# Optimization experiments

Measured on AMD Instinct MI355X. Metric: run time of the kernel, lower is better.

## Reference

```python
import jax, jax.numpy as jnp
import numpy as np

EPS = 1e-06
NEG_SLOPE = 0.2
B, N, CIN = 2, 2048, 64
QK, V, H = 128, 128, 8


def ev_nonlin(x, w1, b1, w2, b2):
    # EVNNonLinearity with skip_connection == 1, leaky_relu
    norm = jnp.linalg.norm(x, axis=-2, keepdims=True)  # [..., 1, nf]
    zero_norm = norm <= EPS
    norm = norm + EPS
    h = jax.nn.leaky_relu(norm @ w1 + b1, NEG_SLOPE)
    norm_bn = (h @ w2 + b2) + norm
    return jnp.where(zero_norm, x, x / norm * norm_bn)


def ev_layernorm(x):
    x_norm = jnp.linalg.norm(x, axis=-2, keepdims=True)
    sigma = jnp.std(jnp.concatenate([x_norm, -x_norm], -1), axis=-1, keepdims=True)
    return x / (sigma + EPS)


def setup_inputs() -> dict:
    key = jax.random.key(0)
    ks = jax.random.split(key, 20)
    def w(k, *shape):
        fan_in = shape[0]
        return jax.random.normal(k, shape, jnp.float32) / np.sqrt(fan_in)
    hd_qk = QK // H
    hd_v = V // H
    return {
        'qfts': jax.random.normal(ks[0], (B, N, 3, CIN), jnp.float32),
        'kvfts': jax.random.normal(ks[1], (B, N, 3, CIN), jnp.float32),
        # EVLinearLeakyReLU for q branch
        'w_q_in': w(ks[2], CIN, QK),
        'q_nl_w1': w(ks[3], QK, QK // 2), 'q_nl_b1': jnp.zeros((QK // 2,), jnp.float32),
        'q_nl_w2': w(ks[4], QK // 2, QK), 'q_nl_b2': jnp.zeros((QK,), jnp.float32),
        # EVLinearLeakyReLU for kv branch
        'w_kv_in': w(ks[5], CIN, QK),
        'kv_nl_w1': w(ks[6], QK, QK // 2), 'kv_nl_b1': jnp.zeros((QK // 2,), jnp.float32),
        'kv_nl_w2': w(ks[7], QK // 2, QK), 'kv_nl_b2': jnp.zeros((QK,), jnp.float32),
        # DenseGeneral projections (no bias)
        'w_q': w(ks[8], QK, H, hd_qk),
        'w_k': w(ks[9], QK, H, hd_qk),
        'w_v': w(ks[10], QK, H, hd_v),
        # output EVLinearLeakyReLU
        'w_out': w(ks[11], V, V),
        'o_nl_w1': w(ks[12], V, V // 2), 'o_nl_b1': jnp.zeros((V // 2,), jnp.float32),
        'o_nl_w2': w(ks[13], V // 2, V), 'o_nl_b2': jnp.zeros((V,), jnp.float32),
    }


def reference(qfts, kvfts, w_q_in, q_nl_w1, q_nl_b1, q_nl_w2, q_nl_b2,
              w_kv_in, kv_nl_w1, kv_nl_b1, kv_nl_w2, kv_nl_b2,
              w_q, w_k, w_v, w_out, o_nl_w1, o_nl_b1, o_nl_w2, o_nl_b2):
    # EVLinearLeakyReLU on q and kv features: [b,n,3,cin] -> [b,n,3,qk]
    qf = ev_nonlin(qfts @ w_q_in, q_nl_w1, q_nl_b1, q_nl_w2, q_nl_b2)
    kf = ev_nonlin(kvfts @ w_kv_in, kv_nl_w1, kv_nl_b1, kv_nl_w2, kv_nl_b2)
    # DenseGeneral to heads, then heads to front: [h,b,n,3,d]
    q = jnp.einsum('bnfc,chd->hbnfd', qf, w_q)
    k = jnp.einsum('bnfc,chd->hbnfd', kf, w_k)
    v = jnp.einsum('bnfc,chd->hbnfd', kf, w_v)
    # normalize_qk
    q = ev_layernorm(q)
    k = ev_layernorm(k)
    # dot attention: contract vector(3) and head_dim axes
    scale = np.sqrt(k.shape[-1]).astype(np.float32)
    attn = jnp.einsum('hbqfd,hbkfd->hbqk', q, k)
    attn = jax.nn.softmax(attn / scale, axis=-1)
    resi = jnp.einsum('hbqk,hbkfd->hbqfd', attn, v)
    # 'h b q f d -> b q f (h d)'
    h, b, nq, f, d = resi.shape
    resi = jnp.moveaxis(resi, 0, 3).reshape(b, nq, f, h * d)
    # output EVLinearLeakyReLU
    out = ev_nonlin(resi @ w_out, o_nl_w1, o_nl_b1, o_nl_w2, o_nl_b2)
    return out
```

## Files before the change

### kernel.cpp

```cpp
#include <hip/hip_runtime.h>
#include <math.h>

#define EPSV 1e-6f
#define NSL  0.2f
#define BB   2
#define NN   2048
#define HH   8
#define TBP  16

typedef short bf16x8 __attribute__((ext_vector_type(8)));
typedef float f32x4  __attribute__((ext_vector_type(4)));

__device__ __forceinline__ unsigned cvt_pk_bf16(float a, float b) {
  unsigned r;
  asm("v_cvt_pk_bf16_f32 %0, %1, %2" : "=v"(r) : "v"(a), "v"(b));
  return r;
}
__device__ __forceinline__ float u2f(unsigned u) {
  union { unsigned u; float f; } v; v.u = u; return v.f;
}
__device__ __forceinline__ float leaky(float a) { return a > 0.f ? a : NSL * a; }

__device__ __forceinline__ void pack8(float4 a, float4 b, uint4& hi, uint4& lo) {
  hi.x = cvt_pk_bf16(a.x, a.y);
  hi.y = cvt_pk_bf16(a.z, a.w);
  hi.z = cvt_pk_bf16(b.x, b.y);
  hi.w = cvt_pk_bf16(b.z, b.w);
  float d0 = a.x - u2f(hi.x << 16), d1 = a.y - u2f(hi.x & 0xffff0000u);
  float d2 = a.z - u2f(hi.y << 16), d3 = a.w - u2f(hi.y & 0xffff0000u);
  float d4 = b.x - u2f(hi.z << 16), d5 = b.y - u2f(hi.z & 0xffff0000u);
  float d6 = b.z - u2f(hi.w << 16), d7 = b.w - u2f(hi.w & 0xffff0000u);
  lo.x = cvt_pk_bf16(d0, d1);
  lo.y = cvt_pk_bf16(d2, d3);
  lo.z = cvt_pk_bf16(d4, d5);
  lo.w = cvt_pk_bf16(d6, d7);
}

__global__ __launch_bounds__(64) void wconv_kernel(
    const float* __restrict__ wq_in, const float* __restrict__ qw1, const float* __restrict__ qw2,
    const float* __restrict__ wkv_in, const float* __restrict__ kw1, const float* __restrict__ kw2,
    const float* __restrict__ w_q, const float* __restrict__ w_k, const float* __restrict__ w_v,
    const float* __restrict__ w_out, const float* __restrict__ ow1, const float* __restrict__ ow2,
    unsigned short* __restrict__ WB)
{
  const int b = blockIdx.x;
  const int lane = threadIdx.x;
  const float* src; int N, toff;
  if      (b < 16)  { src = wq_in;  N = 128; toff = b; }
  else if (b < 32)  { src = qw1;    N = 64;  toff = b - 16; }
  else if (b < 48)  { src = qw2;    N = 128; toff = b - 32; }
  else if (b < 64)  { src = wkv_in; N = 128; toff = b - 48; }
  else if (b < 80)  { src = kw1;    N = 64;  toff = b - 64; }
  else if (b < 96)  { src = kw2;    N = 128; toff = b - 80; }
  else if (b < 128) { src = w_q;    N = 128; toff = b - 96; }
  else if (b < 160) { src = w_k;    N = 128; toff = b - 128; }
  else if (b < 192) { src = w_v;    N = 128; toff = b - 160; }
  else if (b < 224) { src = w_out;  N = 128; toff = b - 192; }
  else if (b < 240) { src = ow1;    N = 64;  toff = b - 224; }
  else              { src = ow2;    N = 128; toff = b - 240; }
  const int NT = N >> 4;
  const int kk = toff / NT, nj = toff % NT;
  const int k0 = kk * 32 + (lane >> 4) * 8;
  const int ch = nj * 16 + (lane & 15);
  float vals[8];
  #pragma unroll
  for (int j = 0; j < 8; ++j) vals[j] = src[(size_t)(k0 + j) * N + ch];
  float4 a = {vals[0], vals[1], vals[2], vals[3]};
  float4 bb = {vals[4], vals[5], vals[6], vals[7]};
  uint4 hi, lo;
  pack8(a, bb, hi, lo);
  unsigned short* dst = WB + (size_t)b * 1024;
  *(uint4*)(dst + lane * 8) = hi;
  *(uint4*)(dst + 512 + lane * 8) = lo;
}


__global__ __launch_bounds__(256) void pre_kernel(
    const float* __restrict__ qfts, const float* __restrict__ kvfts,
    const float* __restrict__ qb1, const float* __restrict__ qb2,
    const float* __restrict__ kb1, const float* __restrict__ kb2,
    const unsigned short* __restrict__ WB,
    unsigned short* __restrict__ QW, unsigned short* __restrict__ KW, unsigned short* __restrict__ VW)
{
  const bool is_kv = blockIdx.y != 0;
  const float* x_in = is_kv ? kvfts : qfts;
  const float* b1 = is_kv ? kb1 : qb1;
  const float* b2 = is_kv ? kb2 : qb2;
  unsigned short* FW = is_kv ? KW : QW;
  const float ln_sc = is_kv ? 1.f : 0.25f * 1.44269504088896f;
  const int tb_in = is_kv ? 48 : 0;
  const int tb_w1 = is_kv ? 64 : 16;
  const int tb_w2 = is_kv ? 80 : 32;
  const int tb_p  = is_kv ? 128 : 96;

  const int t0 = blockIdx.x * TBP;
  const int tid = threadIdx.x;
  const int wv = tid >> 6, lane = tid & 63;
  const int col = lane & 15, kg = lane >> 4;
  const int nj0 = wv * 2;
  const int n0 = t0 & (NN - 1), bsel = t0 >> 11;

  __shared__ __align__(16) char smem[50688];
  float* xs       = (float*)smem;
  float* norm_lds = (float*)(smem + 12544);
  float* h_lds    = (float*)(smem + 20992);
  float* f_lds    = (float*)(smem + 25344);
  float* stage    = (float*)smem;

  {
    const float4* src = (const float4*)(x_in + (size_t)t0 * 192);
    #pragma unroll
    for (int i = 0; i < 3; ++i) {
      int idx = tid + i * 256;
      int row = idx / 48, c4 = idx % 48;
      *(float4*)&xs[row * 196 + c4 * 4] = src[idx];
    }
  }
  __syncthreads();

  f32x4 pacc[3][2];
  #pragma unroll
  for (int mf = 0; mf < 3; ++mf)
    #pragma unroll
    for (int njl = 0; njl < 2; ++njl) pacc[mf][njl] = (f32x4){0.f, 0.f, 0.f, 0.f};
  {
    bf16x8 axh[3][2], axl[3][2];
    #pragma unroll
    for (int mf = 0; mf < 3; ++mf)
      #pragma unroll
      for (int kk = 0; kk < 2; ++kk) {
        const float* pa = &xs[col * 196 + mf * 64 + kk * 32 + kg * 8];
        uint4 hi, lo;
        pack8(*(const float4*)pa, *(const float4*)(pa + 4), hi, lo);
        axh[mf][kk] = *(bf16x8*)&hi; axl[mf][kk] = *(bf16x8*)&lo;
      }
    #pragma unroll
    for (int kk = 0; kk < 2; ++kk)
      #pragma unroll
      for (int njl = 0; njl < 2; ++njl) {
        const unsigned short* wb = WB + (size_t)(tb_in + kk * 8 + nj0 + njl) * 1024 + lane * 8;
        bf16x8 bh = *(const bf16x8*)wb;
        bf16x8 bl = *(const bf16x8*)(wb + 512);
        #pragma unroll
        for (int mf = 0; mf < 3; ++mf) {
          pacc[mf][njl] = __builtin_amdgcn_mfma_f32_16x16x32_bf16(axh[mf][kk], bh, pacc[mf][njl], 0, 0, 0);
          pacc[mf][njl] = __builtin_amdgcn_mfma_f32_16x16x32_bf16(axh[mf][kk], bl, pacc[mf][njl], 0, 0, 0);
          pacc[mf][njl] = __builtin_amdgcn_mfma_f32_16x16x32_bf16(axl[mf][kk], bh, pacc[mf][njl], 0, 0, 0);
        }
      }
  }

  f32x4 np4[2]; int zm = 0;
  #pragma unroll
  for (int njl = 0; njl < 2; ++njl) {
    f32x4 ss = pacc[0][njl] * pacc[0][njl] + pacc[1][njl] * pacc[1][njl] + pacc[2][njl] * pacc[2][njl];
    #pragma unroll
    for (int i = 0; i < 4; ++i) {
      float nn = sqrtf(ss[i]);
      if (nn <= EPSV) zm |= 1 << (njl * 4 + i);
      np4[njl][i] = nn + EPSV;
      norm_lds[(kg * 4 + i) * 132 + (nj0 + njl) * 16 + col] = np4[njl][i];
    }
  }
  __syncthreads();

  {
    f32x4 hacc = {0.f, 0.f, 0.f, 0.f};
    #pragma unroll
    for (int kk = 0; kk < 4; ++kk) {
      const float* pa = &norm_lds[col * 132 + kk * 32 + kg * 8];
      uint4 hi, lo;
      pack8(*(const float4*)pa, *(const float4*)(pa + 4), hi, lo);
      bf16x8 ah = *(bf16x8*)&hi, al = *(bf16x8*)&lo;
      const unsigned short* wb = WB + (size_t)(tb_w1 + kk * 4 + wv) * 1024 + lane * 8;
      bf16x8 bh = *(const bf16x8*)wb, bl = *(const bf16x8*)(wb + 512);
      hacc = __builtin_amdgcn_mfma_f32_16x16x32_bf16(ah, bh, hacc, 0, 0, 0);
      hacc = __builtin_amdgcn_mfma_f32_16x16x32_bf16(ah, bl, hacc, 0, 0, 0);
      hacc = __builtin_amdgcn_mfma_f32_16x16x32_bf16(al, bh, hacc, 0, 0, 0);
    }
    float b1v = b1[wv * 16 + col];
    #pragma unroll
    for (int i = 0; i < 4; ++i)
      h_lds[(kg * 4 + i) * 68 + wv * 16 + col] = leaky(hacc[i] + b1v);
  }
  __syncthreads();

  {
    f32x4 bna[2] = {{0.f, 0.f, 0.f, 0.f}, {0.f, 0.f, 0.f, 0.f}};
    #pragma unroll
    for (int kk = 0; kk < 2; ++kk) {
      const float* pa = &h_lds[col * 68 + kk * 32 + kg * 8];
      uint4 hi, lo;
      pack8(*(const float4*)pa, *(const float4*)(pa + 4), hi, lo);
      bf16x8 ah = *(bf16x8*)&hi, al = *(bf16x8*)&lo;
      #pragma unroll
      for (int njl = 0; njl < 2; ++njl) {
        const unsigned short* wb = WB + (size_t)(tb_w2 + kk * 8 + nj0 + njl) * 1024 + lane * 8;
        bf16x8 bh = *(const bf16x8*)wb, bl = *(const bf16x8*)(wb + 512);
        bna[njl] = __builtin_amdgcn_mfma_f32_16x16x32_bf16(ah, bh, bna[njl], 0, 0, 0);
        bna[njl] = __builtin_amdgcn_mfma_f32_16x16x32_bf16(ah, bl, bna[njl], 0, 0, 0);
        bna[njl] = __builtin_amdgcn_mfma_f32_16x16x32_bf16(al, bh, bna[njl], 0, 0, 0);
      }
    }
    #pragma unroll
    for (int njl = 0; njl < 2; ++njl) {
      float b2v = b2[(nj0 + njl) * 16 + col];
      #pragma unroll
      for (int i = 0; i < 4; ++i) {
        float r = (zm >> (njl * 4 + i)) & 1 ? 1.f
                 : (bna[njl][i] + b2v + np4[njl][i]) / np4[njl][i];
        #pragma unroll
        for (int mf = 0; mf < 3; ++mf)
          f_lds[(mf * 16 + kg * 4 + i) * 132 + (nj0 + njl) * 16 + col] = pacc[mf][njl][i] * r;
      }
    }
  }
  __syncthreads();

  f32x4 qacc[3][2], vacc[3][2];
  #pragma unroll
  for (int mf = 0; mf < 3; ++mf)
    #pragma unroll
    for (int njl = 0; njl < 2; ++njl) {
      qacc[mf][njl] = (f32x4){0.f, 0.f, 0.f, 0.f};
      vacc[mf][njl] = (f32x4){0.f, 0.f, 0.f, 0.f};
    }
  #pragma unroll
  for (int kk = 0; kk < 4; ++kk) {
    bf16x8 afh[3], afl[3];
    #pragma unroll
    for (int mf = 0; mf < 3; ++mf) {
      const float* pa = &f_lds[(mf * 16 + col) * 132 + kk * 32 + kg * 8];
      uint4 hi, lo;
      pack8(*(const float4*)pa, *(const float4*)(pa + 4), hi, lo);
      afh[mf] = *(bf16x8*)&hi; afl[mf] = *(bf16x8*)&lo;
    }
    #pragma unroll
    for (int njl = 0; njl < 2; ++njl) {
      const unsigned short* wbq = WB + (size_t)(tb_p + kk * 8 + nj0 + njl) * 1024 + lane * 8;
      bf16x8 qbh = *(const bf16x8*)wbq, qbl = *(const bf16x8*)(wbq + 512);
      #pragma unroll
      for (int mf = 0; mf < 3; ++mf) {
        qacc[mf][njl] = __builtin_amdgcn_mfma_f32_16x16x32_bf16(afh[mf], qbh, qacc[mf][njl], 0, 0, 0);
        qacc[mf][njl] = __builtin_amdgcn_mfma_f32_16x16x32_bf16(afh[mf], qbl, qacc[mf][njl], 0, 0, 0);
        qacc[mf][njl] = __builtin_amdgcn_mfma_f32_16x16x32_bf16(afl[mf], qbh, qacc[mf][njl], 0, 0, 0);
      }
      if (is_kv) {
        const unsigned short* wbv = WB + (size_t)(160 + kk * 8 + nj0 + njl) * 1024 + lane * 8;
        bf16x8 vbh = *(const bf16x8*)wbv, vbl = *(const bf16x8*)(wbv + 512);
        #pragma unroll
        for (int mf = 0; mf < 3; ++mf) {
          vacc[mf][njl] = __builtin_amdgcn_mfma_f32_16x16x32_bf16(afh[mf], vbh, vacc[mf][njl], 0, 0, 0);
          vacc[mf][njl] = __builtin_amdgcn_mfma_f32_16x16x32_bf16(afh[mf], vbl, vacc[mf][njl], 0, 0, 0);
          vacc[mf][njl] = __builtin_amdgcn_mfma_f32_16x16x32_bf16(afl[mf], vbh, vacc[mf][njl], 0, 0, 0);
        }
      }
    }
  }
  __syncthreads();

  #pragma unroll
  for (int njl = 0; njl < 2; ++njl) {
    #pragma unroll
    for (int i = 0; i < 4; ++i) {
      float ss = qacc[0][njl][i] * qacc[0][njl][i]
               + qacc[1][njl][i] * qacc[1][njl][i]
               + qacc[2][njl][i] * qacc[2][njl][i];
      ss += __shfl_xor(ss, 1, 16);
      ss += __shfl_xor(ss, 2, 16);
      ss += __shfl_xor(ss, 4, 16);
      ss += __shfl_xor(ss, 8, 16);
      float inv = ln_sc / (sqrtf(ss * (1.f / 16.f)) + EPSV);
      const int tl = kg * 4 + i;
      #pragma unroll
      for (int mf = 0; mf < 3; ++mf)
        stage[tl * 388 + mf * 128 + (nj0 + njl) * 16 + col] = qacc[mf][njl][i] * inv;
    }
  }
  __syncthreads();

  {
    const int f0 = lane >> 5;
    const int ddb = ((lane >> 4) & 1) * 8;
    const int row = lane & 15;
    #pragma unroll
    for (int h2 = 0; h2 < 2; ++h2) {
      const int hh = wv * 2 + h2;
      const int hbw = hh * BB + bsel;
      const size_t basew = (size_t)(hbw * 128 + (n0 >> 4)) * 1536;
      {
        const float* p0 = stage + row * 388 + f0 * 128 + hh * 16 + ddb;
        uint4 hi, lo;
        pack8(*(const float4*)p0, *(const float4*)(p0 + 4), hi, lo);
        *(uint4*)(FW + basew + lane * 8) = hi;
        *(uint4*)(FW + basew + 768 + lane * 8) = lo;
      }
      if (lane < 32) {
        const float* p1 = stage + row * 388 + 2 * 128 + hh * 16 + ddb;
        uint4 hi, lo;
        pack8(*(const float4*)p1, *(const float4*)(p1 + 4), hi, lo);
        *(uint4*)(FW + basew + 512 + lane * 8) = hi;
        *(uint4*)(FW + basew + 768 + 512 + lane * 8) = lo;
      }
    }
  }

  if (is_kv) {
    __syncthreads();
    #pragma unroll
    for (int njl = 0; njl < 2; ++njl)
      #pragma unroll
      for (int mf = 0; mf < 3; ++mf)
        #pragma unroll
        for (int i = 0; i < 4; ++i)
          stage[mf * 2112 + (kg * 4 + i) * 132 + (nj0 + njl) * 16 + col] = vacc[mf][njl][i];
    __syncthreads();

    const int s0 = (n0 >> 3) & 3;
    if (lane < 32) {
      const int seg = lane;
      const int tlb = (seg >> 4) * 8;
      const int dd = seg & 15;
      #pragma unroll
      for (int h2 = 0; h2 < 2; ++h2) {
        const int hh = wv * 2 + h2;
        const int hbw = hh * BB + bsel;
        #pragma unroll
        for (int f = 0; f < 3; ++f) {
          const size_t vbase = (size_t)((hbw * 64 + (n0 >> 5)) * 3 + f) * 1024;
          float vals[8];
          #pragma unroll
          for (int j = 0; j < 8; ++j)
            vals[j] = stage[f * 2112 + (tlb + j) * 132 + hh * 16 + dd];
          float4 a = {vals[0], vals[1], vals[2], vals[3]};
          float4 b = {vals[4], vals[5], vals[6], vals[7]};
          uint4 hi, lo;
          pack8(a, b, hi, lo);
          *(uint4*)(VW + vbase + (size_t)(s0 * 16 + seg) * 8) = hi;
          *(uint4*)(VW + vbase + 512 + (size_t)(s0 * 16 + seg) * 8) = lo;
        }
      }
    }
  }
}

#define THR 10.0f

__global__ __launch_bounds__(512, 4) void attn_kernel(
    const unsigned short* __restrict__ QW, const unsigned short* __restrict__ KW,
    const unsigned short* __restrict__ VW, float* __restrict__ Ob)
{
  const int lane = threadIdx.x & 63;
  const int w = threadIdx.x >> 6;
  const int qt = w & 1;
  const int kq = w >> 1;
  const int hb = blockIdx.y;
  const int tA = blockIdx.x * 4 + qt * 2;
  const int q = lane & 15, g = lane >> 4;

  __shared__ unsigned short plds[8][2][1152];
  float* comb = (float*)plds;

  bf16x8 qh0[2], ql0[2], qh1[2], ql1[2];
  #pragma unroll
  for (int qs = 0; qs < 2; ++qs) {
    const size_t qbase = (size_t)(hb * 128 + tA + qs) * 1536;
    qh0[qs] = *(const bf16x8*)(QW + qbase + lane * 8);
    ql0[qs] = *(const bf16x8*)(QW + qbase + 768 + lane * 8);
    qh1[qs] = (bf16x8){0,0,0,0,0,0,0,0};
    ql1[qs] = (bf16x8){0,0,0,0,0,0,0,0};
    if (lane < 32) {
      qh1[qs] = *(const bf16x8*)(QW + qbase + 512 + lane * 8);
      ql1[qs] = *(const bf16x8*)(QW + qbase + 768 + 512 + lane * 8);
    }
  }

  f32x4 o[2][3];
  #pragma unroll
  for (int qs = 0; qs < 2; ++qs)
    #pragma unroll
    for (int f = 0; f < 3; ++f) o[qs][f] = (f32x4){0.f, 0.f, 0.f, 0.f};
  float m[2] = {-INFINITY, -INFINITY}, l[2] = {0.f, 0.f};

  for (int T = kq * 8; T < kq * 8 + 8; ++T) {
    f32x4 sc[2][4];
    __builtin_amdgcn_s_setprio(1);
    #pragma unroll
    for (int st = 0; st < 4; ++st) {
      const size_t kb = (size_t)(hb * 128 + T * 4 + st) * 1536;
      bf16x8 kh0 = *(const bf16x8*)(KW + kb + lane * 8);
      bf16x8 kl0 = *(const bf16x8*)(KW + kb + 768 + lane * 8);
      bf16x8 kh1 = *(const bf16x8*)(KW + kb + 512 + lane * 8);
      bf16x8 kl1 = *(const bf16x8*)(KW + kb + 768 + 512 + lane * 8);
      #pragma unroll
      for (int qs = 0; qs < 2; ++qs) {
        f32x4 a = {0.f, 0.f, 0.f, 0.f};
        a = __builtin_amdgcn_mfma_f32_16x16x32_bf16(kh0, qh0[qs], a, 0, 0, 0);
        a = __builtin_amdgcn_mfma_f32_16x16x32_bf16(kh0, ql0[qs], a, 0, 0, 0);
        a = __builtin_amdgcn_mfma_f32_16x16x32_bf16(kl0, qh0[qs], a, 0, 0, 0);
        a = __builtin_amdgcn_mfma_f32_16x16x32_bf16(kh1, qh1[qs], a, 0, 0, 0);
        a = __builtin_amdgcn_mfma_f32_16x16x32_bf16(kh1, ql1[qs], a, 0, 0, 0);
        a = __builtin_amdgcn_mfma_f32_16x16x32_bf16(kl1, qh1[qs], a, 0, 0, 0);
        sc[qs][st] = a;
      }
    }
    __builtin_amdgcn_s_setprio(0);

    bf16x8 v0h[3], v0l[3];
    {
      const int kc0 = T * 2;
      #pragma unroll
      for (int f = 0; f < 3; ++f) {
        const size_t vb = (size_t)((hb * 64 + kc0) * 3 + f) * 1024;
        v0h[f] = *(const bf16x8*)(VW + vb + lane * 8);
        v0l[f] = *(const bf16x8*)(VW + vb + 512 + lane * 8);
      }
    }

    #pragma unroll
    for (int qs = 0; qs < 2; ++qs) {
      float tm = sc[qs][0][0];
      #pragma unroll
      for (int st = 0; st < 4; ++st)
        #pragma unroll
        for (int r = 0; r < 4; ++r) tm = fmaxf(tm, sc[qs][st][r]);
      tm = fmaxf(tm, __shfl_xor(tm, 16));
      tm = fmaxf(tm, __shfl_xor(tm, 32));
      if (__any(tm > m[qs] + THR)) {
        float mnew = fmaxf(m[qs], tm);
        float scl = __builtin_amdgcn_exp2f(m[qs] - mnew);
        l[qs] *= scl;
        #pragma unroll
        for (int f = 0; f < 3; ++f) {
          o[qs][f][0] *= scl; o[qs][f][1] *= scl;
          o[qs][f][2] *= scl; o[qs][f][3] *= scl;
        }
        m[qs] = mnew;
      }
      float lp = 0.f;
      #pragma unroll
      for (int st = 0; st < 4; ++st) {
        float p0 = __builtin_amdgcn_exp2f(sc[qs][st][0] - m[qs]);
        float p1 = __builtin_amdgcn_exp2f(sc[qs][st][1] - m[qs]);
        float p2 = __builtin_amdgcn_exp2f(sc[qs][st][2] - m[qs]);
        float p3 = __builtin_amdgcn_exp2f(sc[qs][st][3] - m[qs]);
        lp += (p0 + p1) + (p2 + p3);
        uint2 uh = {cvt_pk_bf16(p0, p1), cvt_pk_bf16(p2, p3)};
        *(uint2*)&plds[w][qs][q * 72 + st * 16 + g * 4] = uh;
      }
      lp += __shfl_xor(lp, 16);
      lp += __shfl_xor(lp, 32);
      l[qs] += lp;
    }

    asm volatile("s_waitcnt lgkmcnt(0)" ::: "memory");

    __builtin_amdgcn_s_setprio(1);
    {
      bf16x8 pb[2];
      #pragma unroll
      for (int qs = 0; qs < 2; ++qs)
        pb[qs] = *(const bf16x8*)&plds[w][qs][q * 72 + g * 8];
      #pragma unroll
      for (int f = 0; f < 3; ++f)
        #pragma unroll
        for (int qs = 0; qs < 2; ++qs) {
          o[qs][f] = __builtin_amdgcn_mfma_f32_16x16x32_bf16(v0h[f], pb[qs], o[qs][f], 0, 0, 0);
          o[qs][f] = __builtin_amdgcn_mfma_f32_16x16x32_bf16(v0l[f], pb[qs], o[qs][f], 0, 0, 0);
        }
    }
    {
      const int kc = T * 2 + 1;
      bf16x8 pb[2];
      #pragma unroll
      for (int qs = 0; qs < 2; ++qs)
        pb[qs] = *(const bf16x8*)&plds[w][qs][q * 72 + 32 + g * 8];
      #pragma unroll
      for (int f = 0; f < 3; ++f) {
        const size_t vb = (size_t)((hb * 64 + kc) * 3 + f) * 1024;
        bf16x8 vh = *(const bf16x8*)(VW + vb + lane * 8);
        bf16x8 vl = *(const bf16x8*)(VW + vb + 512 + lane * 8);
        #pragma unroll
        for (int qs = 0; qs < 2; ++qs) {
          o[qs][f] = __builtin_amdgcn_mfma_f32_16x16x32_bf16(vh, pb[qs], o[qs][f], 0, 0, 0);
          o[qs][f] = __builtin_amdgcn_mfma_f32_16x16x32_bf16(vl, pb[qs], o[qs][f], 0, 0, 0);
        }
      }
    }
    __builtin_amdgcn_s_setprio(0);
  }

  #define SLOT(qt_, qs_, r_) (comb + ((((qt_) * 2 + (qs_)) * 2 + (r_)) * 64 + lane) * 14)
  __syncthreads();
  if (kq & 1) {
    #pragma unroll
    for (int qs = 0; qs < 2; ++qs) {
      float* cb = SLOT(qt, qs, kq >> 1);
      #pragma unroll
      for (int f = 0; f < 3; ++f)
        #pragma unroll
        for (int r = 0; r < 4; ++r) cb[f * 4 + r] = o[qs][f][r];
      cb[12] = m[qs]; cb[13] = l[qs];
    }
  }
  __syncthreads();
  if (!(kq & 1)) {
    #pragma unroll
    for (int qs = 0; qs < 2; ++qs) {
      const float* cb = SLOT(qt, qs, kq >> 1);
      float m1 = cb[12], l1 = cb[13];
      float mn = fmaxf(m[qs], m1);
      float s0 = __builtin_amdgcn_exp2f(m[qs] - mn);
      float s1 = __builtin_amdgcn_exp2f(m1 - mn);
      l[qs] = l[qs] * s0 + l1 * s1;
      #pragma unroll
      for (int f = 0; f < 3; ++f)
        #pragma unroll
        for (int r = 0; r < 4; ++r)
          o[qs][f][r] = o[qs][f][r] * s0 + cb[f * 4 + r] * s1;
      m[qs] = mn;
    }
  }
  __syncthreads();
  if (kq == 2) {
    #pragma unroll
    for (int qs = 0; qs < 2; ++qs) {
      float* cb = SLOT(qt, qs, 1);
      #pragma unroll
      for (int f = 0; f < 3; ++f)
        #pragma unroll
        for (int r = 0; r < 4; ++r) cb[f * 4 + r] = o[qs][f][r];
      cb[12] = m[qs]; cb[13] = l[qs];
    }
  }
  __syncthreads();
  if (kq == 0) {
    const int h_ = hb >> 1, b_ = hb & 1;
    #pragma unroll
    for (int qs = 0; qs < 2; ++qs) {
      const float* cb = SLOT(qt, qs, 1);
      float m1 = cb[12], l1 = cb[13];
      float mn = fmaxf(m[qs], m1);
      float s0 = __builtin_amdgcn_exp2f(m[qs] - mn);
      float s1 = __builtin_amdgcn_exp2f(m1 - mn);
      float invl = 1.f / (l[qs] * s0 + l1 * s1);
      const int n = (tA + qs) * 16 + q;
      #pragma unroll
      for (int f = 0; f < 3; ++f) {
        float4 st4 = {(o[qs][f][0] * s0 + cb[f * 4 + 0] * s1) * invl,
                      (o[qs][f][1] * s0 + cb[f * 4 + 1] * s1) * invl,
                      (o[qs][f][2] * s0 + cb[f * 4 + 2] * s1) * invl,
                      (o[qs][f][3] * s0 + cb[f * 4 + 3] * s1) * invl};
        *(float4*)&Ob[(((size_t)(b_ * NN + n)) * 3 + f) * 128 + h_ * 16 + g * 4] = st4;
      }
    }
  }
  #undef SLOT
}

__global__ __launch_bounds__(256) void out_kernel(
    const float* __restrict__ Ob,
    const float* __restrict__ b1, const float* __restrict__ b2,
    const unsigned short* __restrict__ WB,
    float* __restrict__ out)
{
  const int t0 = blockIdx.x * TBP;
  const int tid = threadIdx.x;
  const int wv = tid >> 6, lane = tid & 63;
  const int col = lane & 15, kg = lane >> 4;
  const int nj0 = wv * 2;

  __shared__ __align__(16) char smem[38144];
  float* rs_lds   = (float*)smem;
  float* norm_lds = (float*)(smem + 25344);
  float* h_lds    = (float*)(smem + 33792);
  float* stage    = (float*)smem;

  {
    const float4* src = (const float4*)(Ob + (size_t)t0 * 384);
    #pragma unroll
    for (int i = 0; i < 6; ++i) {
      int idx = tid + i * 256;
      int tok = idx / 96, rem = idx % 96;
      int f = rem / 32, c4 = rem % 32;
      *(float4*)&rs_lds[f * 2112 + tok * 132 + c4 * 4] = src[idx];
    }
  }
  __syncthreads();

  f32x4 pacc[3][2];
  #pragma unroll
  for (int mf = 0; mf < 3; ++mf)
    #pragma unroll
    for (int njl = 0; njl < 2; ++njl) pacc[mf][njl] = (f32x4){0.f, 0.f, 0.f, 0.f};
  #pragma unroll
  for (int kk = 0; kk < 4; ++kk) {
    bf16x8 ah[3], al[3];
    #pragma unroll
    for (int mf = 0; mf < 3; ++mf) {
      const float* pa = &rs_lds[mf * 2112 + col * 132 + kk * 32 + kg * 8];
      uint4 hi, lo;
      pack8(*(const float4*)pa, *(const float4*)(pa + 4), hi, lo);
      ah[mf] = *(bf16x8*)&hi; al[mf] = *(bf16x8*)&lo;
    }
    #pragma unroll
    for (int njl = 0; njl < 2; ++njl) {
      const unsigned short* wb = WB + (size_t)(192 + kk * 8 + nj0 + njl) * 1024 + lane * 8;
      bf16x8 bh = *(const bf16x8*)wb, bl = *(const bf16x8*)(wb + 512);
      #pragma unroll
      for (int mf = 0; mf < 3; ++mf) {
        pacc[mf][njl] = __builtin_amdgcn_mfma_f32_16x16x32_bf16(ah[mf], bh, pacc[mf][njl], 0, 0, 0);
        pacc[mf][njl] = __builtin_amdgcn_mfma_f32_16x16x32_bf16(ah[mf], bl, pacc[mf][njl], 0, 0, 0);
        pacc[mf][njl] = __builtin_amdgcn_mfma_f32_16x16x32_bf16(al[mf], bh, pacc[mf][njl], 0, 0, 0);
      }
    }
  }

  f32x4 np4[2]; int zm = 0;
  #pragma unroll
  for (int njl = 0; njl < 2; ++njl) {
    f32x4 ss = pacc[0][njl] * pacc[0][njl] + pacc[1][njl] * pacc[1][njl] + pacc[2][njl] * pacc[2][njl];
    #pragma unroll
    for (int i = 0; i < 4; ++i) {
      float nn = sqrtf(ss[i]);
      if (nn <= EPSV) zm |= 1 << (njl * 4 + i);
      np4[njl][i] = nn + EPSV;
      norm_lds[(kg * 4 + i) * 132 + (nj0 + njl) * 16 + col] = np4[njl][i];
    }
  }
  __syncthreads();

  {
    f32x4 hacc = {0.f, 0.f, 0.f, 0.f};
    #pragma unroll
    for (int kk = 0; kk < 4; ++kk) {
      const float* pa = &norm_lds[col * 132 + kk * 32 + kg * 8];
      uint4 hi, lo;
      pack8(*(const float4*)pa, *(const float4*)(pa + 4), hi, lo);
      bf16x8 ah = *(bf16x8*)&hi, al = *(bf16x8*)&lo;
      const unsigned short* wb = WB + (size_t)(224 + kk * 4 + wv) * 1024 + lane * 8;
      bf16x8 bh = *(const bf16x8*)wb, bl = *(const bf16x8*)(wb + 512);
      hacc = __builtin_amdgcn_mfma_f32_16x16x32_bf16(ah, bh, hacc, 0, 0, 0);
      hacc = __builtin_amdgcn_mfma_f32_16x16x32_bf16(ah, bl, hacc, 0, 0, 0);
      hacc = __builtin_amdgcn_mfma_f32_16x16x32_bf16(al, bh, hacc, 0, 0, 0);
    }
    float b1v = b1[wv * 16 + col];
    #pragma unroll
    for (int i = 0; i < 4; ++i)
      h_lds[(kg * 4 + i) * 68 + wv * 16 + col] = leaky(hacc[i] + b1v);
  }
  __syncthreads();

  {
    f32x4 bna[2] = {{0.f, 0.f, 0.f, 0.f}, {0.f, 0.f, 0.f, 0.f}};
    #pragma unroll
    for (int kk = 0; kk < 2; ++kk) {
      const float* pa = &h_lds[col * 68 + kk * 32 + kg * 8];
      uint4 hi, lo;
      pack8(*(const float4*)pa, *(const float4*)(pa + 4), hi, lo);
      bf16x8 ah = *(bf16x8*)&hi, al = *(bf16x8*)&lo;
      #pragma unroll
      for (int njl = 0; njl < 2; ++njl) {
        const unsigned short* wb = WB + (size_t)(240 + kk * 8 + nj0 + njl) * 1024 + lane * 8;
        bf16x8 bh = *(const bf16x8*)wb, bl = *(const bf16x8*)(wb + 512);
        bna[njl] = __builtin_amdgcn_mfma_f32_16x16x32_bf16(ah, bh, bna[njl], 0, 0, 0);
        bna[njl] = __builtin_amdgcn_mfma_f32_16x16x32_bf16(ah, bl, bna[njl], 0, 0, 0);
        bna[njl] = __builtin_amdgcn_mfma_f32_16x16x32_bf16(al, bh, bna[njl], 0, 0, 0);
      }
    }
    __syncthreads();
    #pragma unroll
    for (int njl = 0; njl < 2; ++njl) {
      float b2v = b2[(nj0 + njl) * 16 + col];
      #pragma unroll
      for (int i = 0; i < 4; ++i) {
        float r = (zm >> (njl * 4 + i)) & 1 ? 1.f
                 : (bna[njl][i] + b2v + np4[njl][i]) / np4[njl][i];
        #pragma unroll
        for (int mf = 0; mf < 3; ++mf)
          stage[(kg * 4 + i) * 388 + mf * 128 + (nj0 + njl) * 16 + col] = pacc[mf][njl][i] * r;
      }
    }
  }
  __syncthreads();

  {
    float4* dst = (float4*)(out + (size_t)t0 * 384);
    #pragma unroll
    for (int i = 0; i < 6; ++i) {
      int idx = tid + i * 256;
      int tok = idx / 96, rem = idx % 96;
      dst[idx] = *(const float4*)&stage[tok * 388 + rem * 4];
    }
  }
}

extern "C" void kernel_launch(void* const* d_in, const int* in_sizes, int n_in,
                              void* d_out, int out_size, void* d_ws, size_t ws_size,
                              hipStream_t stream) {
  const float* qfts   = (const float*)d_in[0];
  const float* kvfts  = (const float*)d_in[1];
  const float* w_q_in = (const float*)d_in[2];
  const float* q_w1   = (const float*)d_in[3];
  const float* q_b1   = (const float*)d_in[4];
  const float* q_w2   = (const float*)d_in[5];
  const float* q_b2   = (const float*)d_in[6];
  const float* w_kv_in= (const float*)d_in[7];
  const float* kv_w1  = (const float*)d_in[8];
  const float* kv_b1  = (const float*)d_in[9];
  const float* kv_w2  = (const float*)d_in[10];
  const float* kv_b2  = (const float*)d_in[11];
  const float* w_q    = (const float*)d_in[12];
  const float* w_k    = (const float*)d_in[13];
  const float* w_v    = (const float*)d_in[14];
  const float* w_out  = (const float*)d_in[15];
  const float* o_w1   = (const float*)d_in[16];
  const float* o_b1   = (const float*)d_in[17];
  const float* o_w2   = (const float*)d_in[18];
  const float* o_b2   = (const float*)d_in[19];

  unsigned short* QW = (unsigned short*)d_ws;
  unsigned short* KW = QW + 3145728;
  unsigned short* VW = KW + 3145728;
  float* Obuf = (float*)(VW + 3145728);
  unsigned short* WB = (unsigned short*)(Obuf + 1572864);

  wconv_kernel<<<256, 64, 0, stream>>>(w_q_in, q_w1, q_w2, w_kv_in, kv_w1, kv_w2,
                                       w_q, w_k, w_v, w_out, o_w1, o_w2, WB);
  dim3 pg(BB * NN / TBP, 2);
  pre_kernel<<<pg, 256, 0, stream>>>(qfts, kvfts, q_b1, q_b2, kv_b1, kv_b2,
                                     WB, QW, KW, VW);
  dim3 ag(32, 16);
  attn_kernel<<<ag, 512, 0, stream>>>(QW, KW, VW, Obuf);
  out_kernel<<<BB * NN / TBP, 256, 0, stream>>>(Obuf, o_b1, o_b2, WB, (float*)d_out);
}
```

Measured before the change: 81.63 us.

## Remap attention blocks to XCDs by head-batch and drop early V prefetch

Block indices are remapped so that consecutive block ids, which are dealt round-robin across the eight XCDs, put all query tiles of one head-batch pair on the same XCD. Each XCD's L2 then holds the K/V data for only two head-batch pairs. The early register prefetch of the first V chunk, issued before the softmax, is removed and both V chunks are now loaded inside a unified loop. This lowers register pressure but exposes V load latency right next to the MFMAs that use it.

Result: no change. 80.80 us (median of 2 runs) (-1.0%).

```diff
diff --git a/kernel.cpp b/kernel.cpp
--- a/kernel.cpp
+++ b/kernel.cpp
@@ -354,8 +354,11 @@
   const int w = threadIdx.x >> 6;
   const int qt = w & 1;
   const int kq = w >> 1;
-  const int hb = blockIdx.y;
-  const int tA = blockIdx.x * 4 + qt * 2;
+  const int fid = blockIdx.y * 32 + blockIdx.x;
+  const int xcd = fid & 7, slot = fid >> 3;
+  const int hb = xcd * 2 + (slot >> 5);
+  const int bx = slot & 31;
+  const int tA = bx * 4 + qt * 2;
   const int q = lane & 15, g = lane >> 4;
 
   __shared__ unsigned short plds[8][2][1152];
@@ -406,17 +409,6 @@
     }
     __builtin_amdgcn_s_setprio(0);
 
-    bf16x8 v0h[3], v0l[3];
-    {
-      const int kc0 = T * 2;
-      #pragma unroll
-      for (int f = 0; f < 3; ++f) {
-        const size_t vb = (size_t)((hb * 64 + kc0) * 3 + f) * 1024;
-        v0h[f] = *(const bf16x8*)(VW + vb + lane * 8);
-        v0l[f] = *(const bf16x8*)(VW + vb + 512 + lane * 8);
-      }
-    }
-
     #pragma unroll
     for (int qs = 0; qs < 2; ++qs) {
       float tm = sc[qs][0][0];
@@ -456,25 +448,13 @@
     asm volatile("s_waitcnt lgkmcnt(0)" ::: "memory");
 
     __builtin_amdgcn_s_setprio(1);
-    {
+    #pragma unroll
+    for (int c = 0; c < 2; ++c) {
+      const int kc = T * 2 + c;
       bf16x8 pb[2];
       #pragma unroll
       for (int qs = 0; qs < 2; ++qs)
-        pb[qs] = *(const bf16x8*)&plds[w][qs][q * 72 + g * 8];
-      #pragma unroll
-      for (int f = 0; f < 3; ++f)
-        #pragma unroll
-        for (int qs = 0; qs < 2; ++qs) {
-          o[qs][f] = __builtin_amdgcn_mfma_f32_16x16x32_bf16(v0h[f], pb[qs], o[qs][f], 0, 0, 0);
-          o[qs][f] = __builtin_amdgcn_mfma_f32_16x16x32_bf16(v0l[f], pb[qs], o[qs][f], 0, 0, 0);
-        }
-    }
-    {
-      const int kc = T * 2 + 1;
-      bf16x8 pb[2];
-      #pragma unroll
-      for (int qs = 0; qs < 2; ++qs)
-        pb[qs] = *(const bf16x8*)&plds[w][qs][q * 72 + 32 + g * 8];
+        pb[qs] = *(const bf16x8*)&plds[w][qs][q * 72 + c * 32 + g * 8];
       #pragma unroll
       for (int f = 0; f < 3; ++f) {
         const size_t vb = (size_t)((hb * 64 + kc) * 3 + f) * 1024;
```
